# Optimization experiments

Measured on AMD Instinct MI355X. Metric: run time of the kernel, lower is better.

The kernel has to match this reference:

```python
import jax, jax.numpy as jnp
import numpy as np

DEGREE = 3          # bspline_array passes t_dim positionally as degree
C_DIM = 64          # coefficients per spline
N_SPLINES = 64      # n
T_DIM = C_DIM + DEGREE + 1   # knots per spline = 68
BATCH = 65536


def setup_inputs() -> dict:
    key = jax.random.key(0)
    k1, k2, k3 = jax.random.split(key, 3)
    x = jax.random.normal(k1, (BATCH, N_SPLINES), dtype=jnp.float32)
    t = jax.random.normal(k2, (N_SPLINES, T_DIM), dtype=jnp.float32)   # knot vectors (learned, unsorted as in source)
    c = jax.random.normal(k3, (N_SPLINES, C_DIM), dtype=jnp.float32)   # control coefficients
    return {"x": x, "t": t, "c": c}


def _safe_div(num, den):
    # Cox-de Boor convention: 0/0 := 0 (handles repeated knots)
    zero = den == 0
    return jnp.where(zero, 0.0, num / jnp.where(zero, 1.0, den))


def cox_deboor_batched(t, c, x):
    """Vectorized Cox-de Boor over all n splines and the whole batch.

    t: [n, T_DIM] knots, c: [n, C_DIM] coeffs, x: [B, n] -> out [B, n]
    """
    xe = x[..., None]                                   # [B, n, 1]
    # degree-0 basis: indicator t_i <= x < t_{i+1}      # [B, n, T_DIM-1]
    N = ((t[:, :-1] <= xe) & (xe < t[:, 1:])).astype(x.dtype)
    for k in range(1, DEGREE + 1):
        m = T_DIM - 1 - k
        left = _safe_div(xe - t[:, :m], t[:, k:k + m] - t[:, :m]) * N[..., :m]
        right = _safe_div(t[:, k + 1:k + 1 + m] - xe,
                          t[:, k + 1:k + 1 + m] - t[:, 1:1 + m]) * N[..., 1:1 + m]
        N = left + right                                # [B, n, m]
    # S(x) = sum_i c_i * B_{i,p}(x)
    return jnp.einsum('bni,ni->bn', N[..., :C_DIM], c)  # [B, n]


def reference(x, t, c):
    return cox_deboor_batched(t, c, x)
```

## Files before the change

### kernel.cpp

```cpp
#include <hip/hip_runtime.h>

#define BATCH 65536
#define NSPL  64
#define CDIM  64
#define TDIM  68
#define QI    67
#define RTN   67

#define TCOLS 16
#define TROWS 256
#define NTHR  256
#define PITCH 257


__global__ __launch_bounds__(128) void prep(const float* __restrict__ T,
                                            const float* __restrict__ C,
                                            float4* __restrict__ RT) {
    __shared__ double  td[TDIM];
    __shared__ double  cd[CDIM];
    __shared__ double  R1[QI], R2[TDIM - 2], R3[TDIM - 3];
    __shared__ double4 Qd[QI];
    __shared__ float   tf[TDIM];
    __shared__ float   srt[TDIM];

    const int s = blockIdx.x;
    const int t = threadIdx.x;

    if (t < TDIM) { float v = T[s * TDIM + t]; tf[t] = v; td[t] = (double)v; }
    if (t >= 64 && t < 64 + CDIM) cd[t - 64] = (double)C[s * CDIM + t - 64];
    __syncthreads();

    if (t < TDIM - 1) { double d = td[t + 1] - td[t]; R1[t] = (d == 0.0) ? 0.0 : 1.0 / d; }
    if (t < TDIM - 2) { double d = td[t + 2] - td[t]; R2[t] = (d == 0.0) ? 0.0 : 1.0 / d; }
    if (t < TDIM - 3) { double d = td[t + 3] - td[t]; R3[t] = (d == 0.0) ? 0.0 : 1.0 / d; }
    if (t < TDIM) {
        float v = tf[t];
        int r = 0;
        for (int k = 0; k < TDIM; ++k)
            r += (tf[k] < v) || (tf[k] == v && k < t);
        srt[r] = v;
    }
    __syncthreads();

    if (t < QI) {
        const int i = t;
        double q0 = 0, q1 = 0, q2 = 0, q3 = 0;
        for (int j = i - 3; j <= i; ++j) {
            if (j < 0 || j > CDIM - 1) continue;
            double cj = cd[j];
            for (int b2 = 0; b2 < 2; ++b2) {
                int m2 = j + b2;
                double D3 = R3[j + b2];
                double p3 = b2 ? -D3 : D3;
                double r3 = b2 ? D3 * td[j + 4] : -D3 * td[j];
                for (int b1 = 0; b1 < 2; ++b1) {
                    int m1 = m2 + b1;
                    double D2 = R2[m2 + b1];
                    double p2 = b1 ? -D2 : D2;
                    double r2 = b1 ? D2 * td[m2 + 3] : -D2 * td[m2];
                    for (int b0 = 0; b0 < 2; ++b0) {
                        if (m1 + b0 != i) continue;
                        double D1 = R1[m1 + b0];
                        double p1 = b0 ? -D1 : D1;
                        double r1 = b0 ? D1 * td[m1 + 2] : -D1 * td[m1];
                        double a2 = p3 * p2, a1 = p3 * r2 + r3 * p2, a0 = r3 * r2;
                        q3 += cj * (a2 * p1);
                        q2 += cj * (a2 * r1 + a1 * p1);
                        q1 += cj * (a1 * r1 + a0 * p1);
                        q0 += cj * (a0 * r1);
                    }
                }
            }
        }
        double4 q; q.x = q0; q.y = q1; q.z = q2; q.w = q3;
        Qd[i] = q;
    }
    __syncthreads();

    if (t >= 1 && t <= RTN) {
        const float xs = srt[t - 1];
        double a0 = 0, a1 = 0, a2 = 0, a3 = 0;
        for (int i = 0; i < QI; ++i) {
            if (tf[i] <= xs && xs < tf[i + 1]) {
                double4 q = Qd[i];
                a0 += q.x; a1 += q.y; a2 += q.z; a3 += q.w;
            }
        }
        float4 v; v.x = (float)a0; v.y = (float)a1; v.z = (float)a2; v.w = (float)a3;
        RT[s * RTN + (t - 1)] = v;
    }
}

static __device__ __forceinline__ float rdlane(float v, int l) {
    return __builtin_bit_cast(float, __builtin_amdgcn_readlane(__builtin_bit_cast(int, v), l));
}

__global__ __launch_bounds__(NTHR) void bspline_main(const float* __restrict__ X,
                                                     const float* __restrict__ T,
                                                     const float4* __restrict__ RT,
                                                     float* __restrict__ O) {
    __shared__ float4 rt[TCOLS * RTN];
    __shared__ float  xl[TCOLS * PITCH];

    const int tid  = threadIdx.x;
    const int lane = tid & 63;
    const int w    = tid >> 6;
    const int r0   = blockIdx.x * TROWS;
    const int s0   = blockIdx.y * TCOLS;

    for (int e = tid; e < TCOLS * RTN; e += NTHR)
        rt[e] = RT[s0 * RTN + e];

    #pragma unroll
    for (int it = 0; it < TROWS * TCOLS / NTHR; ++it) {
        int e = tid + it * NTHR;
        int r = e >> 4, c = e & 15;
        xl[c * PITCH + r] = X[(r0 + r) * NSPL + s0 + c];
    }

    float kA[4], kB[4];
    #pragma unroll
    for (int cc = 0; cc < 4; ++cc) {
        const int sp = s0 + w * 4 + cc;
        kA[cc] = T[sp * TDIM + lane];
        kB[cc] = T[sp * TDIM + 64 + (lane & 3)];
    }
    __syncthreads();

    #pragma unroll 1
    for (int cc = 0; cc < 4; ++cc) {
        const int c = w * 4 + cc;
        float* xc = xl + c * PITCH + lane;

        float x0 = xc[0], x1 = xc[64], x2 = xc[128], x3 = xc[192];
        unsigned n0 = 0, n1 = 0, n2 = 0, n3 = 0;

        #pragma unroll
        for (int j = 0; j < 64; ++j) {
            float tj = rdlane(kA[cc], j);
            n0 += (x0 >= tj); n1 += (x1 >= tj);
            n2 += (x2 >= tj); n3 += (x3 >= tj);
        }
        #pragma unroll
        for (int j = 0; j < 4; ++j) {
            float tj = rdlane(kB[cc], j);
            n0 += (x0 >= tj); n1 += (x1 >= tj);
            n2 += (x2 >= tj); n3 += (x3 >= tj);
        }

        const int m0 = (n0 < 1u ? 0 : (n0 > 67u ? 66 : (int)n0 - 1));
        const int m1 = (n1 < 1u ? 0 : (n1 > 67u ? 66 : (int)n1 - 1));
        const int m2 = (n2 < 1u ? 0 : (n2 > 67u ? 66 : (int)n2 - 1));
        const int m3 = (n3 < 1u ? 0 : (n3 > 67u ? 66 : (int)n3 - 1));
        float4 p0 = rt[c * RTN + m0];
        float4 p1 = rt[c * RTN + m1];
        float4 p2 = rt[c * RTN + m2];
        float4 p3 = rt[c * RTN + m3];
        float y0 = fmaf(fmaf(fmaf(p0.w, x0, p0.z), x0, p0.y), x0, p0.x);
        float y1 = fmaf(fmaf(fmaf(p1.w, x1, p1.z), x1, p1.y), x1, p1.x);
        float y2 = fmaf(fmaf(fmaf(p2.w, x2, p2.z), x2, p2.y), x2, p2.x);
        float y3 = fmaf(fmaf(fmaf(p3.w, x3, p3.z), x3, p3.y), x3, p3.x);
        y0 = (n0 - 1u < 67u) ? y0 : 0.f;
        y1 = (n1 - 1u < 67u) ? y1 : 0.f;
        y2 = (n2 - 1u < 67u) ? y2 : 0.f;
        y3 = (n3 - 1u < 67u) ? y3 : 0.f;

        xc[0] = y0; xc[64] = y1; xc[128] = y2; xc[192] = y3;
    }
    __syncthreads();

    #pragma unroll
    for (int it = 0; it < TROWS * TCOLS / NTHR; ++it) {
        int e = tid + it * NTHR;
        int r = e >> 4, c = e & 15;
        O[(r0 + r) * NSPL + s0 + c] = xl[c * PITCH + r];
    }
}

extern "C" void kernel_launch(void* const* d_in, const int* in_sizes, int n_in,
                              void* d_out, int out_size, void* d_ws, size_t ws_size,
                              hipStream_t stream) {
    const float* X = (const float*)d_in[0];
    const float* T = (const float*)d_in[1];
    const float* C = (const float*)d_in[2];
    float* O = (float*)d_out;
    float4* RT = (float4*)d_ws;

    prep<<<NSPL, 128, 0, stream>>>(T, C, RT);
    dim3 grid(BATCH / TROWS, NSPL / TCOLS);
    bspline_main<<<grid, NTHR, 0, stream>>>(X, T, RT, O);
}
```

Baseline: 103.9 us.

## Halve row tile, drop shared coefficient table, gather directly from global

The row tile per block shrinks from 256 to 128, doubling the grid. The per-block copy of the per-spline polynomial table into shared memory is removed, and coefficients are gathered straight from global memory (L1/L2 cached). The count loop is restructured to interleave all four splines per wave, which adds independent work per knot broadcast. The aim is to cut shared-memory traffic and the staging cost per block and to raise occupancy, at the cost of scattered global gathers.

Result: no change. 103.7 us (-0.2%).

```diff
diff --git a/kernel.cpp b/kernel.cpp
--- a/kernel.cpp
+++ b/kernel.cpp
@@ -8,9 +8,9 @@
 #define RTN   67
 
 #define TCOLS 16
-#define TROWS 256
+#define TROWS 128
 #define NTHR  256
-#define PITCH 257
+#define PITCH 129
 
 
 __global__ __launch_bounds__(128) void prep(const float* __restrict__ T,
@@ -99,17 +99,13 @@
                                                      const float* __restrict__ T,
                                                      const float4* __restrict__ RT,
                                                      float* __restrict__ O) {
-    __shared__ float4 rt[TCOLS * RTN];
-    __shared__ float  xl[TCOLS * PITCH];
+    __shared__ float xl[TCOLS * PITCH];
 
     const int tid  = threadIdx.x;
     const int lane = tid & 63;
     const int w    = tid >> 6;
     const int r0   = blockIdx.x * TROWS;
     const int s0   = blockIdx.y * TCOLS;
-
-    for (int e = tid; e < TCOLS * RTN; e += NTHR)
-        rt[e] = RT[s0 * RTN + e];
 
     #pragma unroll
     for (int it = 0; it < TROWS * TCOLS / NTHR; ++it) {
@@ -127,45 +123,54 @@
     }
     __syncthreads();
 
-    #pragma unroll 1
+    float    xv0[4], xv1[4];
+    unsigned n0[4], n1[4];
+    #pragma unroll
     for (int cc = 0; cc < 4; ++cc) {
-        const int c = w * 4 + cc;
-        float* xc = xl + c * PITCH + lane;
+        const float* xc = xl + (w * 4 + cc) * PITCH + lane;
+        xv0[cc] = xc[0];
+        xv1[cc] = xc[64];
+        n0[cc] = 0; n1[cc] = 0;
+    }
 
-        float x0 = xc[0], x1 = xc[64], x2 = xc[128], x3 = xc[192];
-        unsigned n0 = 0, n1 = 0, n2 = 0, n3 = 0;
+    #pragma unroll
+    for (int j = 0; j < 64; ++j) {
+        #pragma unroll
+        for (int cc = 0; cc < 4; ++cc) {
+            float tj = rdlane(kA[cc], j);
+            n0[cc] += (xv0[cc] >= tj);
+            n1[cc] += (xv1[cc] >= tj);
+        }
+    }
+    #pragma unroll
+    for (int j = 0; j < 4; ++j) {
+        #pragma unroll
+        for (int cc = 0; cc < 4; ++cc) {
+            float tj = rdlane(kB[cc], j);
+            n0[cc] += (xv0[cc] >= tj);
+            n1[cc] += (xv1[cc] >= tj);
+        }
+    }
 
+    #pragma unroll
+    for (int half = 0; half < 2; ++half) {
+        float*    xvp = half ? xv1 : xv0;
+        unsigned* np  = half ? n1  : n0;
+        float4 p[4];
         #pragma unroll
-        for (int j = 0; j < 64; ++j) {
-            float tj = rdlane(kA[cc], j);
-            n0 += (x0 >= tj); n1 += (x1 >= tj);
-            n2 += (x2 >= tj); n3 += (x3 >= tj);
+        for (int cc = 0; cc < 4; ++cc) {
+            unsigned i = np[cc] - 1u;
+            i = (i > 66u) ? 66u : i;
+            const int sp = s0 + w * 4 + cc;
+            p[cc] = RT[sp * RTN + i];
         }
         #pragma unroll
-        for (int j = 0; j < 4; ++j) {
-            float tj = rdlane(kB[cc], j);
-            n0 += (x0 >= tj); n1 += (x1 >= tj);
-            n2 += (x2 >= tj); n3 += (x3 >= tj);
+        for (int cc = 0; cc < 4; ++cc) {
+            float x = xvp[cc];
+            float y = fmaf(fmaf(fmaf(p[cc].w, x, p[cc].z), x, p[cc].y), x, p[cc].x);
+            y = (np[cc] - 1u < 67u) ? y : 0.f;
+            xl[(w * 4 + cc) * PITCH + lane + (half ? 64 : 0)] = y;
         }
-
-        const int m0 = (n0 < 1u ? 0 : (n0 > 67u ? 66 : (int)n0 - 1));
-        const int m1 = (n1 < 1u ? 0 : (n1 > 67u ? 66 : (int)n1 - 1));
-        const int m2 = (n2 < 1u ? 0 : (n2 > 67u ? 66 : (int)n2 - 1));
-        const int m3 = (n3 < 1u ? 0 : (n3 > 67u ? 66 : (int)n3 - 1));
-        float4 p0 = rt[c * RTN + m0];
-        float4 p1 = rt[c * RTN + m1];
-        float4 p2 = rt[c * RTN + m2];
-        float4 p3 = rt[c * RTN + m3];
-        float y0 = fmaf(fmaf(fmaf(p0.w, x0, p0.z), x0, p0.y), x0, p0.x);
-        float y1 = fmaf(fmaf(fmaf(p1.w, x1, p1.z), x1, p1.y), x1, p1.x);
-        float y2 = fmaf(fmaf(fmaf(p2.w, x2, p2.z), x2, p2.y), x2, p2.x);
-        float y3 = fmaf(fmaf(fmaf(p3.w, x3, p3.z), x3, p3.y), x3, p3.x);
-        y0 = (n0 - 1u < 67u) ? y0 : 0.f;
-        y1 = (n1 - 1u < 67u) ? y1 : 0.f;
-        y2 = (n2 - 1u < 67u) ? y2 : 0.f;
-        y3 = (n3 - 1u < 67u) ? y3 : 0.f;
-
-        xc[0] = y0; xc[64] = y1; xc[128] = y2; xc[192] = y3;
     }
     __syncthreads();
 
```
